# Kernel tuning notes

Hardware: AMD Instinct MI355X
Metric: run time of the kernel (lower is better)

The kernel has to match this reference:

```python
import jax, jax.numpy as jnp
import numpy as np

B, H, N, C = 4, 8, 2048, 32
N_SCALAR, N_VEC = 16, 4  # attn_reps = '16x0n+4x1n' -> C = 16 + 4*4 = 32
ETA = jnp.array([1.0, -1.0, -1.0, -1.0], dtype=jnp.float32)  # Minkowski metric diag


def _frame_transform(x, M):
    """Apply per-particle 4x4 matrix M to the vector channels of x.

    x: (B, H, N, C) with layout [16 scalars | 4 four-vectors]
    M: (B, N, 4, 4), shared across heads (module repeats frames over heads).
    """
    s = x[..., :N_SCALAR]                                   # (B,H,N,16) untouched
    v = x[..., N_SCALAR:].reshape(x.shape[:-1] + (N_VEC, 4))  # (B,H,N,4,4)
    v = jnp.einsum('bnij,bhnvj->bhnvi', M, v)
    return jnp.concatenate([s, v.reshape(x.shape[:-1] + (N_VEC * 4,))], axis=-1)


def setup_inputs() -> dict:
    key = jax.random.key(0)
    kq, kk, kv, kf = jax.random.split(key, 4)
    q = jax.random.normal(kq, (B, H, N, C), dtype=jnp.float32)
    k = jax.random.normal(kk, (B, H, N, C), dtype=jnp.float32)
    v = jax.random.normal(kv, (B, H, N, C), dtype=jnp.float32)
    # Genuine Lorentz frames: identity time component + random spatial rotation.
    A = jax.random.normal(kf, (B, N, 3, 3), dtype=jnp.float32)
    Q, _ = jnp.linalg.qr(A)  # (B,N,3,3) orthogonal
    frames = jnp.zeros((B, N, 4, 4), dtype=jnp.float32)
    frames = frames.at[..., 0, 0].set(1.0).at[..., 1:, 1:].set(Q)
    return {'q_local': q, 'k_local': k, 'v_local': v, 'frames': frames}


def reference(q_local, k_local, v_local, frames):
    # Inverse Lorentz frame: L^{-1} = eta L^T eta ; index-lowered inverse = L^T.
    frames_T = jnp.swapaxes(frames, -1, -2)                 # (B,N,4,4)
    inv = frames_T * ETA[:, None] * ETA[None, :]            # eta L^T eta
    lower_inv = frames_T
    # 1) local -> global frame
    q_g = _frame_transform(q_local, inv)
    k_g = _frame_transform(k_local, lower_inv)
    v_g = _frame_transform(v_local, inv)
    # 2) muP-scaled attention (1/d, not 1/sqrt(d))
    scores = jnp.einsum('bhqc,bhkc->bhqk', q_g, k_g) * (1.0 / C)
    weights = jax.nn.softmax(scores, axis=-1)
    out_g = jnp.einsum('bhqk,bhkc->bhqc', weights, v_g)
    # 3) global -> local frame
    return _frame_transform(out_g, frames)
```

## Files before the change

### kernel.cpp

```cpp
#include <hip/hip_runtime.h>
#include <hip/hip_bf16.h>


#define NB 4
#define NH 8
#define NS 2048
#define NC 32

typedef float f32x4 __attribute__((ext_vector_type(4)));
typedef short s16x8 __attribute__((ext_vector_type(8)));
typedef short s16x4 __attribute__((ext_vector_type(4)));

#define QSCALE 0.04511260931463978f

__device__ __forceinline__ short f2bf(float f) {
  union { float f; unsigned u; } c; c.f = f;
  return (short)((c.u + 0x7FFFu + ((c.u >> 16) & 1u)) >> 16);
}

__device__ __forceinline__ void gload16(const void* g, void* l) {
  __builtin_amdgcn_global_load_lds(
      (const __attribute__((address_space(1))) unsigned int*)g,
      (__attribute__((address_space(3))) unsigned int*)l, 16, 0, 0);
}

__device__ __forceinline__ void load_Q3(const float* __restrict__ F, int b, int n,
                                        float q9[9]) {
  const float* p = F + ((size_t)(b * NS + n)) * 16 + 5;
  q9[0] = p[0]; q9[1] = p[1]; q9[2] = p[2];
  q9[3] = p[4]; q9[4] = p[5]; q9[5] = p[6];
  q9[6] = p[8]; q9[7] = p[9]; q9[8] = p[10];
}

__device__ __forceinline__ void rotT(const float q9[9], f32x4& v) {
  const float x = v[1], y = v[2], z = v[3];
  v[1] = q9[0] * x + q9[3] * y + q9[6] * z;
  v[2] = q9[1] * x + q9[4] * y + q9[7] * z;
  v[3] = q9[2] * x + q9[5] * y + q9[8] * z;
}

__device__ __forceinline__ void rotF(const float q9[9], f32x4& v) {
  const float x = v[1], y = v[2], z = v[3];
  v[1] = q9[0] * x + q9[1] * y + q9[2] * z;
  v[2] = q9[3] * x + q9[4] * y + q9[5] * z;
  v[3] = q9[6] * x + q9[7] * y + q9[8] * z;
}

__launch_bounds__(256)
__global__ void rot_cast(const float* __restrict__ Kg,
                         const float* __restrict__ Vg,
                         const float* __restrict__ Fg,
                         unsigned short* __restrict__ Kbf,
                         unsigned short* __restrict__ Vt) {
  const int gid = blockIdx.x * 256 + threadIdx.x;
  if (gid < 65536) {
    const int r = gid;
    const int n = r & (NS - 1);
    const int b = r >> 14;
    const float* p = Kg + (size_t)r * NC;
    f32x4 c[8];
#pragma unroll
    for (int i = 0; i < 8; i++) c[i] = *(const f32x4*)(p + 4 * i);
    float q9[9]; load_Q3(Fg, b, n, q9);
#pragma unroll
    for (int i = 4; i < 8; i++) rotT(q9, c[i]);
    unsigned short* o = Kbf + (size_t)r * NC;
    const int ks = n & 3;
#pragma unroll
    for (int i = 0; i < 8; i += 2) {
      s16x8 w;
#pragma unroll
      for (int e = 0; e < 4; e++) {
        w[e]     = f2bf(c[i][e]);
        w[4 + e] = f2bf(c[i + 1][e]);
      }
      *(s16x8*)(o + (((i >> 1) ^ ks) << 3)) = w;
    }
  } else {
    const int r  = gid - 65536;
    const int bh = r >> 9;
    const int b  = bh >> 3;
    const int K0 = (r & 511) << 2;
    const float* vsrc = Vg + ((size_t)bh * NS + K0) * NC;
    s16x4 outc[32];
#pragma unroll
    for (int k = 0; k < 4; k++) {
      f32x4 c[8];
#pragma unroll
      for (int i = 0; i < 8; i++) c[i] = *(const f32x4*)(vsrc + (size_t)k * NC + 4 * i);
      float q9[9]; load_Q3(Fg, b, K0 + k, q9);
#pragma unroll
      for (int i = 4; i < 8; i++) rotT(q9, c[i]);
#pragma unroll
      for (int i = 0; i < 8; i++)
#pragma unroll
        for (int e = 0; e < 4; e++) outc[i * 4 + e][k] = f2bf(c[i][e]);
    }
    const int cg     = K0 & 31;
    const int sub4   = cg >> 2;
    const int newsub = (sub4 & 3) * 2 + (sub4 >> 2);
    const int pos    = ((K0 & 127) >> 5) * 32 + newsub * 4;
    const int gpos   = pos >> 3;
    const int rem    = pos & 7;
    unsigned short* ob = Vt + (size_t)bh * (NS * NC) + ((K0 >> 7) & 15) * 4096;
#pragma unroll
    for (int ch = 0; ch < 32; ch++)
      *(s16x4*)(ob + ch * 128 + ((gpos ^ (ch & 15)) << 3) + rem) = outc[ch];
  }
}

__launch_bounds__(256, 2)
__global__ void lloca_attn(const float* __restrict__ Qg,
                           const unsigned short* __restrict__ Kbf,
                           const unsigned short* __restrict__ Vt,
                           const float* __restrict__ Fg,
                           float* __restrict__ Og) {
  __shared__ __align__(16) unsigned short Klds[2][256 * 32];
  __shared__ __align__(16) unsigned short Vlds[2][2 * 32 * 128];

  const int tid  = threadIdx.x;
  const int lane = tid & 63;
  const int wv   = tid >> 6;
  const int g    = lane >> 4;
  const int lq   = lane & 15;

  const int bid = blockIdx.x;
  const int blk = (bid & 7) * 64 + (bid >> 3);
  const int b   = blk >> 7;
  const int h   = (blk >> 4) & 7;
  const int qb  = blk & 15;

  const size_t bhr = (size_t)(b * NH + h) * NS;
  const unsigned short* Kp  = Kbf + bhr * NC;
  const unsigned short* Vtp = Vt  + bhr * NC;
  float*                Op  = Og  + bhr * NC;

  const int qbase = qb * 128 + wv * 32;

  const f32x4 zero4 = {0.f, 0.f, 0.f, 0.f};
  const short ONE = (short)0x3F80;
  const s16x8 ones8 = {ONE, ONE, ONE, ONE, ONE, ONE, ONE, ONE};

  s16x8 qfrag[2];
  f32x4 acc[2][2];
  f32x4 accL[2];
#pragma unroll
  for (int t = 0; t < 2; t++) {
    const int qi = qbase + t * 16 + lq;
    const float* qp = Qg + (bhr + qi) * NC + g * 8;
    f32x4 a = *(const f32x4*)qp;
    f32x4 c = *(const f32x4*)(qp + 4);
    if (g >= 2) {
      float q9[9]; load_Q3(Fg, b, qi, q9);
      rotT(q9, a);
      rotT(q9, c);
    }
#pragma unroll
    for (int e = 0; e < 4; e++) {
      qfrag[t][e]     = f2bf(a[e] * QSCALE);
      qfrag[t][4 + e] = f2bf(c[e] * QSCALE);
    }
    acc[t][0] = zero4;
    acc[t][1] = zero4;
    accL[t]   = zero4;
  }

  const int lel = lane * 8;

#define STAGE(buf, i)                                                          \
  do {                                                                         \
    const size_t goff = (size_t)(i) * 8192;                                    \
    const unsigned short* ks = Kp + goff + wv * 2048 + lel;                    \
    const unsigned short* vs = Vtp + goff + wv * 2048 + lel;                   \
    unsigned short* kd = &Klds[buf][wv * 2048];                                \
    unsigned short* vd = &Vlds[buf][wv * 2048];                                \
    gload16(ks, kd);               gload16(ks + 512, kd + 512);                \
    gload16(ks + 1024, kd + 1024); gload16(ks + 1536, kd + 1536);              \
    gload16(vs, vd);               gload16(vs + 512, vd + 512);                \
    gload16(vs + 1024, vd + 1024); gload16(vs + 1536, vd + 1536);              \
  } while (0)

  STAGE(0, 0);

  const int ksw = (g ^ (lq & 3)) << 3;

  const int NTT = NS / 256;
  for (int i = 0; i < NTT; i++) {
    const int cur = i & 1;
    asm volatile("s_waitcnt vmcnt(0)" ::: "memory");
    __builtin_amdgcn_s_barrier();
    __builtin_amdgcn_sched_barrier(0);
    if (i + 1 < NTT) STAGE(cur ^ 1, i + 1);
    __builtin_amdgcn_s_setprio(1);
#pragma unroll
    for (int kgi = 0; kgi < 8; kgi++) {
      const int kgb = kgi * 32;
      const s16x8 kf0 = *(const s16x8*)&Klds[cur][(kgb + lq) * 32 + ksw];
      const s16x8 kf1 = *(const s16x8*)&Klds[cur][(kgb + 16 + lq) * 32 + ksw];
      const int vbase2 = (kgb >> 7) * 4096;
      const int kgb7   = kgb & 127;
      const int vsw    = ((((kgb7) >> 3) + g) ^ lq) << 3;
      const s16x8 va0 = *(const s16x8*)&Vlds[cur][vbase2 + lq * 128 + vsw];
      const s16x8 va1 = *(const s16x8*)&Vlds[cur][vbase2 + (16 + lq) * 128 + vsw];
#pragma unroll
      for (int t = 0; t < 2; t++) {
        f32x4 s0 = __builtin_amdgcn_mfma_f32_16x16x32_bf16(kf0, qfrag[t], zero4, 0, 0, 0);
        f32x4 s1 = __builtin_amdgcn_mfma_f32_16x16x32_bf16(kf1, qfrag[t], zero4, 0, 0, 0);
        float p0 = __builtin_amdgcn_exp2f(s0[0]);
        float p1 = __builtin_amdgcn_exp2f(s0[1]);
        float p2 = __builtin_amdgcn_exp2f(s0[2]);
        float p3 = __builtin_amdgcn_exp2f(s0[3]);
        float p4 = __builtin_amdgcn_exp2f(s1[0]);
        float p5 = __builtin_amdgcn_exp2f(s1[1]);
        float p6 = __builtin_amdgcn_exp2f(s1[2]);
        float p7 = __builtin_amdgcn_exp2f(s1[3]);
        union { __hip_bfloat162 h2v[4]; s16x8 v; } pk;
        pk.h2v[0] = __float22bfloat162_rn(make_float2(p0, p1));
        pk.h2v[1] = __float22bfloat162_rn(make_float2(p2, p3));
        pk.h2v[2] = __float22bfloat162_rn(make_float2(p4, p5));
        pk.h2v[3] = __float22bfloat162_rn(make_float2(p6, p7));
        accL[t]   = __builtin_amdgcn_mfma_f32_16x16x32_bf16(ones8, pk.v, accL[t], 0, 0, 0);
        acc[t][0] = __builtin_amdgcn_mfma_f32_16x16x32_bf16(va0,   pk.v, acc[t][0], 0, 0, 0);
        acc[t][1] = __builtin_amdgcn_mfma_f32_16x16x32_bf16(va1,   pk.v, acc[t][1], 0, 0, 0);
      }
    }
    __builtin_amdgcn_s_setprio(0);
  }

#pragma unroll
  for (int t = 0; t < 2; t++) {
    const float inv = 1.0f / accL[t][0];
    const int qi = qbase + t * 16 + lq;
    float* op = Op + (size_t)qi * NC;
    f32x4 o0, o1;
#pragma unroll
    for (int r = 0; r < 4; r++) {
      o0[r] = acc[t][0][r] * inv;
      o1[r] = acc[t][1][r] * inv;
    }
    float q9[9]; load_Q3(Fg, b, qi, q9);
    rotF(q9, o1);
    *(f32x4*)(op + g * 4)      = o0;
    *(f32x4*)(op + 16 + g * 4) = o1;
  }
}

extern "C" void kernel_launch(void* const* d_in, const int* in_sizes, int n_in,
                              void* d_out, int out_size, void* d_ws, size_t ws_size,
                              hipStream_t stream) {
  (void)in_sizes; (void)n_in; (void)ws_size; (void)out_size;
  const float* q = (const float*)d_in[0];
  const float* k = (const float*)d_in[1];
  const float* v = (const float*)d_in[2];
  const float* f = (const float*)d_in[3];
  float* o = (float*)d_out;

  const size_t NEL = (size_t)NB * NH * NS * NC;
  unsigned short* kbf = (unsigned short*)d_ws;
  unsigned short* vt  = kbf + NEL;

  hipLaunchKernelGGL(rot_cast, dim3(320), dim3(256), 0, stream,
                     k, v, f, kbf, vt);
  hipLaunchKernelGGL(lloca_attn, dim3(512), dim3(256), 0, stream,
                     q, kbf, vt, f, o);
}
```

Before: 40.17 us.

## Double per-wave query tile to 64 rows and rebalance the rot_cast work split

The attention kernel now gives each wave 64 query rows (four 16-row tiles) instead of 32, halving the grid to 256 blocks, with launch bounds set to one block per SM. Each K/V fragment loaded from LDS is reused across twice as many queries, which cuts LDS traffic and the number of staging passes over K/V. In exchange, register pressure rises and there are fewer blocks to hide latency, since 256 blocks roughly match the CU count. The rot_cast kernel also changes its mapping: each K thread handles two rows, and each V thread handles two keys, writing 32-bit stores into the transposed layout instead of 64-bit ones.

```diff
diff --git a/kernel.cpp b/kernel.cpp
--- a/kernel.cpp
+++ b/kernel.cpp
@@ -53,63 +53,69 @@
                          unsigned short* __restrict__ Kbf,
                          unsigned short* __restrict__ Vt) {
   const int gid = blockIdx.x * 256 + threadIdx.x;
-  if (gid < 65536) {
-    const int r = gid;
-    const int n = r & (NS - 1);
-    const int b = r >> 14;
-    const float* p = Kg + (size_t)r * NC;
-    f32x4 c[8];
-#pragma unroll
-    for (int i = 0; i < 8; i++) c[i] = *(const f32x4*)(p + 4 * i);
-    float q9[9]; load_Q3(Fg, b, n, q9);
-#pragma unroll
-    for (int i = 4; i < 8; i++) rotT(q9, c[i]);
-    unsigned short* o = Kbf + (size_t)r * NC;
-    const int ks = n & 3;
-#pragma unroll
-    for (int i = 0; i < 8; i += 2) {
-      s16x8 w;
-#pragma unroll
-      for (int e = 0; e < 4; e++) {
-        w[e]     = f2bf(c[i][e]);
-        w[4 + e] = f2bf(c[i + 1][e]);
+  if (gid < 32768) {
+#pragma unroll
+    for (int rr = 0; rr < 2; rr++) {
+      const int r = 2 * gid + rr;
+      const int n = r & (NS - 1);
+      const int b = r >> 14;
+      const float* p = Kg + (size_t)r * NC;
+      f32x4 c[8];
+#pragma unroll
+      for (int i = 0; i < 8; i++) c[i] = *(const f32x4*)(p + 4 * i);
+      float q9[9]; load_Q3(Fg, b, n, q9);
+#pragma unroll
+      for (int i = 4; i < 8; i++) rotT(q9, c[i]);
+      unsigned short* o = Kbf + (size_t)r * NC;
+      const int ks = n & 3;
+#pragma unroll
+      for (int i = 0; i < 8; i += 2) {
+        s16x8 w;
+#pragma unroll
+        for (int e = 0; e < 4; e++) {
+          w[e]     = f2bf(c[i][e]);
+          w[4 + e] = f2bf(c[i + 1][e]);
+        }
+        *(s16x8*)(o + (((i >> 1) ^ ks) << 3)) = w;
       }
-      *(s16x8*)(o + (((i >> 1) ^ ks) << 3)) = w;
     }
   } else {
-    const int r  = gid - 65536;
-    const int bh = r >> 9;
+    const int u  = gid - 32768;
+    const int bh = u >> 10;
     const int b  = bh >> 3;
-    const int K0 = (r & 511) << 2;
+    const int K0 = (u & 1023) << 1;
     const float* vsrc = Vg + ((size_t)bh * NS + K0) * NC;
-    s16x4 outc[32];
-#pragma unroll
-    for (int k = 0; k < 4; k++) {
+    unsigned short o0[32], o1[32];
+#pragma unroll
+    for (int k = 0; k < 2; k++) {
       f32x4 c[8];
 #pragma unroll
       for (int i = 0; i < 8; i++) c[i] = *(const f32x4*)(vsrc + (size_t)k * NC + 4 * i);
       float q9[9]; load_Q3(Fg, b, K0 + k, q9);
 #pragma unroll
       for (int i = 4; i < 8; i++) rotT(q9, c[i]);
+      unsigned short* dst = k ? o1 : o0;
 #pragma unroll
       for (int i = 0; i < 8; i++)
 #pragma unroll
-        for (int e = 0; e < 4; e++) outc[i * 4 + e][k] = f2bf(c[i][e]);
-    }
-    const int cg     = K0 & 31;
-    const int sub4   = cg >> 2;
+        for (int e = 0; e < 4; e++) dst[i * 4 + e] = (unsigned short)f2bf(c[i][e]);
+    }
+    const int c7     = K0 & 127;
+    const int sub4   = (c7 & 31) >> 2;
     const int newsub = (sub4 & 3) * 2 + (sub4 >> 2);
-    const int pos    = ((K0 & 127) >> 5) * 32 + newsub * 4;
+    const int pos    = (c7 >> 5) * 32 + newsub * 4 + (K0 & 3);
     const int gpos   = pos >> 3;
     const int rem    = pos & 7;
-    unsigned short* ob = Vt + (size_t)bh * (NS * NC) + ((K0 >> 7) & 15) * 4096;
-#pragma unroll
-    for (int ch = 0; ch < 32; ch++)
-      *(s16x4*)(ob + ch * 128 + ((gpos ^ (ch & 15)) << 3) + rem) = outc[ch];
-  }
-}
-
-__launch_bounds__(256, 2)
+    unsigned short* ob = Vt + (size_t)bh * (NS * NC) + (K0 >> 7) * 4096;
+#pragma unroll
+    for (int ch = 0; ch < 32; ch++) {
+      unsigned uu = (unsigned)o0[ch] | ((unsigned)o1[ch] << 16);
+      *(unsigned*)(ob + ch * 128 + ((gpos ^ (ch & 15)) << 3) + rem) = uu;
+    }
+  }
+}
+
+__launch_bounds__(256, 1)
 __global__ void lloca_attn(const float* __restrict__ Qg,
                            const unsigned short* __restrict__ Kbf,
                            const unsigned short* __restrict__ Vt,
@@ -125,27 +131,27 @@
   const int lq   = lane & 15;
 
   const int bid = blockIdx.x;
-  const int blk = (bid & 7) * 64 + (bid >> 3);
-  const int b   = blk >> 7;
-  const int h   = (blk >> 4) & 7;
-  const int qb  = blk & 15;
+  const int blk = (bid & 7) * 32 + (bid >> 3);
+  const int b   = blk >> 6;
+  const int h   = (blk >> 3) & 7;
+  const int qb  = blk & 7;
 
   const size_t bhr = (size_t)(b * NH + h) * NS;
   const unsigned short* Kp  = Kbf + bhr * NC;
   const unsigned short* Vtp = Vt  + bhr * NC;
   float*                Op  = Og  + bhr * NC;
 
-  const int qbase = qb * 128 + wv * 32;
+  const int qbase = qb * 256 + wv * 64;
 
   const f32x4 zero4 = {0.f, 0.f, 0.f, 0.f};
   const short ONE = (short)0x3F80;
   const s16x8 ones8 = {ONE, ONE, ONE, ONE, ONE, ONE, ONE, ONE};
 
-  s16x8 qfrag[2];
-  f32x4 acc[2][2];
-  f32x4 accL[2];
-#pragma unroll
-  for (int t = 0; t < 2; t++) {
+  s16x8 qfrag[4];
+  f32x4 acc[4][2];
+  f32x4 accL[4];
+#pragma unroll
+  for (int t = 0; t < 4; t++) {
     const int qi = qbase + t * 16 + lq;
     const float* qp = Qg + (bhr + qi) * NC + g * 8;
     f32x4 a = *(const f32x4*)qp;
@@ -203,7 +209,7 @@
       const s16x8 va0 = *(const s16x8*)&Vlds[cur][vbase2 + lq * 128 + vsw];
       const s16x8 va1 = *(const s16x8*)&Vlds[cur][vbase2 + (16 + lq) * 128 + vsw];
 #pragma unroll
-      for (int t = 0; t < 2; t++) {
+      for (int t = 0; t < 4; t++) {
         f32x4 s0 = __builtin_amdgcn_mfma_f32_16x16x32_bf16(kf0, qfrag[t], zero4, 0, 0, 0);
         f32x4 s1 = __builtin_amdgcn_mfma_f32_16x16x32_bf16(kf1, qfrag[t], zero4, 0, 0, 0);
         float p0 = __builtin_amdgcn_exp2f(s0[0]);
@@ -228,7 +234,7 @@
   }
 
 #pragma unroll
-  for (int t = 0; t < 2; t++) {
+  for (int t = 0; t < 4; t++) {
     const float inv = 1.0f / accL[t][0];
     const int qi = qbase + t * 16 + lq;
     float* op = Op + (size_t)qi * NC;
@@ -259,8 +265,8 @@
   unsigned short* kbf = (unsigned short*)d_ws;
   unsigned short* vt  = kbf + NEL;
 
-  hipLaunchKernelGGL(rot_cast, dim3(320), dim3(256), 0, stream,
+  hipLaunchKernelGGL(rot_cast, dim3(256), dim3(256), 0, stream,
                      k, v, f, kbf, vt);
-  hipLaunchKernelGGL(lloca_attn, dim3(512), dim3(256), 0, stream,
+  hipLaunchKernelGGL(lloca_attn, dim3(256), dim3(256), 0, stream,
                      q, kbf, vt, f, o);
 }
```

Measured after the change: 45.44 us. 1.13x slower.
